# Kernel optimization log

Measured on AMD Instinct MI355X. Metric: run time of the kernel, lower is better.

## Reference

```python
import jax, jax.numpy as jnp
import numpy as np

SIGMA = 1.0

def setup_inputs() -> dict:
    key = jax.random.key(0)
    kx, ky = jax.random.split(key)
    x = jax.random.normal(kx, (8192, 256), dtype=jnp.float32)
    y = jax.random.normal(ky, (8192, 256), dtype=jnp.float32)
    return {"x": x, "y": y}

def reference(x, y):
    x2 = jnp.sum(x * x, axis=-1)            # [N]
    y2 = jnp.sum(y * y, axis=-1)            # [M]
    d2 = x2[:, None] + y2[None, :] - 2.0 * (x @ y.T)  # [N, M]
    d2 = jnp.maximum(d2, 0.0)
    k = jnp.exp(-d2 / (2.0 * SIGMA ** 2))
    # original: exp(...)[None].sum(dim=0).mean() == mean over all N*M entries
    return jnp.mean(k)
```

## Files before the change

### kernel.cpp

```cpp
#include <hip/hip_runtime.h>

#define NROWS 8192
#define DIM   256

typedef __bf16 bf16x8 __attribute__((ext_vector_type(8)));
typedef __bf16 bf16x4 __attribute__((ext_vector_type(4)));
typedef float  f32x4  __attribute__((ext_vector_type(4)));

typedef __attribute__((address_space(3))) char lds_char;
typedef __attribute__((address_space(1))) const char glob_char;

#define LOG2E  1.4426950408889634f
#define NEG_HALF_LOG2E (-0.7213475204444817f)

#define BAR() asm volatile("s_barrier" ::: "memory")

__global__ __launch_bounds__(256) void prep_kernel(
    const float* __restrict__ x, const float* __restrict__ y,
    __bf16* __restrict__ xb, __bf16* __restrict__ yb,
    float* __restrict__ px, float* __restrict__ py,
    float* __restrict__ out)
{
    int tid  = threadIdx.x;
    int lane = tid & 63;
    int w    = tid >> 6;
    int row  = blockIdx.x * 4 + w;
    bool isx = row < NROWS;
    int r    = isx ? row : row - NROWS;
    const float* src = (isx ? x : y) + (size_t)r * DIM;
    float4 v = reinterpret_cast<const float4*>(src)[lane];
    float sq = v.x*v.x + v.y*v.y + v.z*v.z + v.w*v.w;
    #pragma unroll
    for (int off = 32; off; off >>= 1) sq += __shfl_xor(sq, off);
    bf16x4 h;
    h[0] = (__bf16)v.x; h[1] = (__bf16)v.y; h[2] = (__bf16)v.z; h[3] = (__bf16)v.w;
    __bf16* dst = (isx ? xb : yb) + (size_t)r * DIM + lane * 4;
    *reinterpret_cast<bf16x4*>(dst) = h;
    if (lane == 0) (isx ? px : py)[r] = NEG_HALF_LOG2E * sq;
    if (blockIdx.x == 0 && tid == 0) out[0] = 0.0f;
}

__global__ __launch_bounds__(512, 1) void rbf_gemm_kernel(
    const __bf16* __restrict__ xb, const __bf16* __restrict__ yb,
    const float* __restrict__ px, const float* __restrict__ py,
    float* __restrict__ out)
{
    __shared__ char smem[131072];
    __shared__ float red[8];

    int tid  = threadIdx.x;
    int lane = tid & 63;
    int wv   = tid >> 6;
    int wm   = wv >> 2;
    int wn   = wv & 3;
    int bm   = blockIdx.x & 31;
    int bn   = blockIdx.x >> 5;
    int h    = lane >> 4;
    int l15  = lane & 15;

    f32x4 acc[8][4];
    #pragma unroll
    for (int m = 0; m < 8; ++m)
        #pragma unroll
        for (int n = 0; n < 4; ++n)
            acc[m][n] = (f32x4){0.f, 0.f, 0.f, 0.f};

    auto stage_unit = [&](int buf, int kt, int matrix, int unit) {
        const __bf16* src = matrix ? yb : xb;
        int baserow = (matrix ? bn : bm) * 256;
        #pragma unroll
        for (int j = 0; j < 2; ++j) {
            int lin = j * 8192 + tid * 16;
            int off;
            if (matrix == 0) off = unit * 8192 + lin + (lin >> 13) * 8192;
            else             off = unit * 4096 + lin + (lin >> 12) * 4096;
            int row = off >> 7;
            int kb  = off & 127;
            int kbs = kb ^ ((row & 7) << 4);
            size_t g = (size_t)(baserow + row) * 512 + (size_t)kt * 128 + kbs;
            __builtin_amdgcn_global_load_lds(
                (glob_char*)((const char*)src + g),
                (lds_char*)(smem + buf * 65536 + matrix * 32768 + off), 16, 0, 0);
        }
    };

    auto ldA = [&](int buf, int mbase, bf16x8* aF) {
        const char* Ab = smem + buf * 65536;
        #pragma unroll
        for (int m = 0; m < 4; ++m)
            #pragma unroll
            for (int kk = 0; kk < 2; ++kk) {
                int row = wm * 128 + (mbase + m) * 16 + l15;
                int kb  = (kk * 64 + h * 16) ^ ((row & 7) << 4);
                aF[m * 2 + kk] = *reinterpret_cast<const bf16x8*>(Ab + row * 128 + kb);
            }
    };
    auto ldB = [&](int buf, int nbase, bf16x8* bF) {
        const char* Bb = smem + buf * 65536 + 32768;
        #pragma unroll
        for (int n = 0; n < 2; ++n)
            #pragma unroll
            for (int kk = 0; kk < 2; ++kk) {
                int row = wn * 64 + (nbase + n) * 16 + l15;
                int kb  = (kk * 64 + h * 16) ^ ((row & 7) << 4);
                bF[n * 2 + kk] = *reinterpret_cast<const bf16x8*>(Bb + row * 128 + kb);
            }
    };
    auto mmaq = [&](int mbase, int nbase, bf16x8* aF, bf16x8* bF) {
        __builtin_amdgcn_s_setprio(1);
        #pragma unroll
        for (int m = 0; m < 4; ++m)
            #pragma unroll
            for (int n = 0; n < 2; ++n)
                #pragma unroll
                for (int kk = 0; kk < 2; ++kk)
                    acc[mbase + m][nbase + n] = __builtin_amdgcn_mfma_f32_16x16x32_bf16(
                        aF[m * 2 + kk], bF[n * 2 + kk], acc[mbase + m][nbase + n], 0, 0, 0);
        __builtin_amdgcn_s_setprio(0);
    };

    stage_unit(0, 0, 0, 0); stage_unit(0, 0, 1, 0);
    stage_unit(0, 0, 1, 1); stage_unit(0, 0, 0, 1);
    stage_unit(1, 1, 0, 0); stage_unit(1, 1, 1, 0);
    stage_unit(1, 1, 1, 1); stage_unit(1, 1, 0, 1);
    asm volatile("s_waitcnt vmcnt(8)" ::: "memory");
    BAR();

    #pragma unroll
    for (int kt = 0; kt < 4; ++kt) {
        int buf = kt & 1;
        bf16x8 aF[8], bF0[4], bF1[4];
        ldA(buf, 0, aF);
        ldB(buf, 0, bF0);
        mmaq(0, 0, aF, bF0);
        BAR();
        ldB(buf, 2, bF1);
        if (kt < 2) { stage_unit(buf, kt + 2, 0, 0); stage_unit(buf, kt + 2, 1, 0); }
        mmaq(0, 2, aF, bF1);
        BAR();
        ldA(buf, 4, aF);
        if (kt < 2) stage_unit(buf, kt + 2, 1, 1);
        mmaq(4, 2, aF, bF1);
        BAR();
        if (kt < 2) stage_unit(buf, kt + 2, 0, 1);
        mmaq(4, 0, aF, bF0);
        if (kt < 2)       asm volatile("s_waitcnt vmcnt(8)" ::: "memory");
        else if (kt == 2) asm volatile("s_waitcnt vmcnt(0)" ::: "memory");
        BAR();
    }

    float lsum = 0.f;
    int colbase = bn * 256 + wn * 64 + l15;
    int rowbase = bm * 256 + wm * 128 + h * 4;
    float py4[4];
    #pragma unroll
    for (int n = 0; n < 4; ++n) py4[n] = py[colbase + n * 16];
    #pragma unroll
    for (int m = 0; m < 8; ++m) {
        #pragma unroll
        for (int r = 0; r < 4; ++r) {
            float pxv = px[rowbase + m * 16 + r];
            #pragma unroll
            for (int n = 0; n < 4; ++n)
                lsum += exp2f(fmaf(acc[m][n][r], LOG2E, pxv + py4[n]));
        }
    }
    #pragma unroll
    for (int off = 32; off; off >>= 1) lsum += __shfl_xor(lsum, off);
    if (lane == 0) red[wv] = lsum;
    __syncthreads();
    if (tid == 0) {
        float s = (red[0] + red[1] + red[2] + red[3] +
                   red[4] + red[5] + red[6] + red[7]) * 1.4901161193847656e-08f;
        atomicAdd(out, s);
    }
}

extern "C" void kernel_launch(void* const* d_in, const int* in_sizes, int n_in,
                              void* d_out, int out_size, void* d_ws, size_t ws_size,
                              hipStream_t stream) {
    const float* x = (const float*)d_in[0];
    const float* y = (const float*)d_in[1];
    float* out = (float*)d_out;
    char* ws = (char*)d_ws;
    __bf16* xb = (__bf16*)ws;
    __bf16* yb = (__bf16*)(ws + (size_t)4 * 1024 * 1024);
    float*  px = (float*)(ws + (size_t)8 * 1024 * 1024);
    float*  py = (float*)(ws + (size_t)8 * 1024 * 1024 + 32 * 1024);

    hipLaunchKernelGGL(prep_kernel, dim3(4096), dim3(256), 0, stream,
                       x, y, xb, yb, px, py, out);
    hipLaunchKernelGGL(rbf_gemm_kernel, dim3(1024), dim3(512), 0, stream,
                       xb, yb, px, py, out);
}
```

Before: 113.5 us.

## Make GEMM blocks persistent over four N-tiles with cross-tile prefetch

Launches one block per CU (256 blocks), each looping over four consecutive 256-column output tiles for a fixed row block. Global-to-LDS staging of the next tile's first K slices overlaps with the current tile's last MFMA steps, hiding per-block prologue latency. The px/py norm vectors are preloaded into LDS via direct global-to-LDS loads and read vectorized in the epilogue. Epilogue exp work per tile is not overlapped with loads, and the added outer loop may raise register pressure.

```diff
diff --git a/kernel.cpp b/kernel.cpp
--- a/kernel.cpp
+++ b/kernel.cpp
@@ -45,18 +45,21 @@
     const float* __restrict__ px, const float* __restrict__ py,
     float* __restrict__ out)
 {
-    __shared__ char smem[131072];
-    __shared__ float red[8];
+    __shared__ __align__(16) char smem[136224];
+    float* pxl = (float*)(smem + 131072);
+    float* pyl = (float*)(smem + 132096);
+    float* red = (float*)(smem + 136192);
 
     int tid  = threadIdx.x;
     int lane = tid & 63;
     int wv   = tid >> 6;
     int wm   = wv >> 2;
     int wn   = wv & 3;
-    int bm   = blockIdx.x & 31;
-    int bn   = blockIdx.x >> 5;
+    int bm   = blockIdx.x >> 3;
+    int bng  = blockIdx.x & 7;
     int h    = lane >> 4;
     int l15  = lane & 15;
+    int arow = bm * 256;
 
     f32x4 acc[8][4];
     #pragma unroll
@@ -65,9 +68,8 @@
         for (int n = 0; n < 4; ++n)
             acc[m][n] = (f32x4){0.f, 0.f, 0.f, 0.f};
 
-    auto stage_unit = [&](int buf, int kt, int matrix, int unit) {
+    auto stage_unit = [&](int buf, int ktcol, int matrix, int unit, int baserow) {
         const __bf16* src = matrix ? yb : xb;
-        int baserow = (matrix ? bn : bm) * 256;
         #pragma unroll
         for (int j = 0; j < 2; ++j) {
             int lin = j * 8192 + tid * 16;
@@ -75,9 +77,8 @@
             if (matrix == 0) off = unit * 8192 + lin + (lin >> 13) * 8192;
             else             off = unit * 4096 + lin + (lin >> 12) * 4096;
             int row = off >> 7;
-            int kb  = off & 127;
-            int kbs = kb ^ ((row & 7) << 4);
-            size_t g = (size_t)(baserow + row) * 512 + (size_t)kt * 128 + kbs;
+            int kbs = (off & 127) ^ ((row & 7) << 4);
+            size_t g = (size_t)(baserow + row) * 512 + (size_t)ktcol + kbs;
             __builtin_amdgcn_global_load_lds(
                 (glob_char*)((const char*)src + g),
                 (lds_char*)(smem + buf * 65536 + matrix * 32768 + off), 16, 0, 0);
@@ -119,52 +120,73 @@
         __builtin_amdgcn_s_setprio(0);
     };
 
-    stage_unit(0, 0, 0, 0); stage_unit(0, 0, 1, 0);
-    stage_unit(0, 0, 1, 1); stage_unit(0, 0, 0, 1);
-    stage_unit(1, 1, 0, 0); stage_unit(1, 1, 1, 0);
-    stage_unit(1, 1, 1, 1); stage_unit(1, 1, 0, 1);
+    if (tid < 256)
+        __builtin_amdgcn_global_load_lds(
+            (glob_char*)((const char*)(px + arow) + tid * 4),
+            (lds_char*)((char*)pxl + tid * 4), 4, 0, 0);
+    #pragma unroll
+    for (int j = 0; j < 2; ++j)
+        __builtin_amdgcn_global_load_lds(
+            (glob_char*)((const char*)(py + bng * 1024) + j * 2048 + tid * 4),
+            (lds_char*)((char*)pyl + j * 2048 + tid * 4), 4, 0, 0);
+    int bn0row = bng * 4 * 256;
+    stage_unit(0, 0,   0, 0, arow); stage_unit(0, 0,   1, 0, bn0row);
+    stage_unit(0, 0,   1, 1, bn0row); stage_unit(0, 0,   0, 1, arow);
+    stage_unit(1, 128, 0, 0, arow); stage_unit(1, 128, 1, 0, bn0row);
+    stage_unit(1, 128, 1, 1, bn0row); stage_unit(1, 128, 0, 1, arow);
     asm volatile("s_waitcnt vmcnt(8)" ::: "memory");
     BAR();
 
-    #pragma unroll
-    for (int kt = 0; kt < 4; ++kt) {
-        int buf = kt & 1;
-        bf16x8 aF[8], bF0[4], bF1[4];
-        ldA(buf, 0, aF);
-        ldB(buf, 0, bF0);
-        mmaq(0, 0, aF, bF0);
-        BAR();
-        ldB(buf, 2, bF1);
-        if (kt < 2) { stage_unit(buf, kt + 2, 0, 0); stage_unit(buf, kt + 2, 1, 0); }
-        mmaq(0, 2, aF, bF1);
-        BAR();
-        ldA(buf, 4, aF);
-        if (kt < 2) stage_unit(buf, kt + 2, 1, 1);
-        mmaq(4, 2, aF, bF1);
-        BAR();
-        if (kt < 2) stage_unit(buf, kt + 2, 0, 1);
-        mmaq(4, 0, aF, bF0);
-        if (kt < 2)       asm volatile("s_waitcnt vmcnt(8)" ::: "memory");
-        else if (kt == 2) asm volatile("s_waitcnt vmcnt(0)" ::: "memory");
-        BAR();
-    }
-
     float lsum = 0.f;
-    int colbase = bn * 256 + wn * 64 + l15;
-    int rowbase = bm * 256 + wm * 128 + h * 4;
-    float py4[4];
-    #pragma unroll
-    for (int n = 0; n < 4; ++n) py4[n] = py[colbase + n * 16];
-    #pragma unroll
-    for (int m = 0; m < 8; ++m) {
-        #pragma unroll
-        for (int r = 0; r < 4; ++r) {
-            float pxv = px[rowbase + m * 16 + r];
+    for (int t = 0; t < 4; ++t) {
+        #pragma unroll
+        for (int kt = 0; kt < 4; ++kt) {
+            int buf = kt & 1;
+            bool st = (t < 3) || (kt < 2);
+            int tgt_kt  = (kt + 2) & 3;
+            int tgt_col = tgt_kt * 128;
+            int tgt_bnrow = (bng * 4 + t + (kt >> 1)) * 256;
+            bf16x8 aF[8], bF0[4], bF1[4];
+            ldA(buf, 0, aF);
+            ldB(buf, 0, bF0);
+            mmaq(0, 0, aF, bF0);
+            BAR();
+            ldB(buf, 2, bF1);
+            if (st) { stage_unit(buf, tgt_col, 0, 0, arow);
+                      stage_unit(buf, tgt_col, 1, 0, tgt_bnrow); }
+            mmaq(0, 2, aF, bF1);
+            BAR();
+            ldA(buf, 4, aF);
+            if (st) stage_unit(buf, tgt_col, 1, 1, tgt_bnrow);
+            mmaq(4, 2, aF, bF1);
+            BAR();
+            if (st) stage_unit(buf, tgt_col, 0, 1, arow);
+            mmaq(4, 0, aF, bF0);
+            if (st)            asm volatile("s_waitcnt vmcnt(8)" ::: "memory");
+            else if (kt == 2)  asm volatile("s_waitcnt vmcnt(0)" ::: "memory");
+            BAR();
+        }
+        float py4[4];
+        #pragma unroll
+        for (int n = 0; n < 4; ++n)
+            py4[n] = pyl[t * 256 + wn * 64 + n * 16 + l15];
+        #pragma unroll
+        for (int m = 0; m < 8; ++m) {
+            f32x4 pxm = *reinterpret_cast<const f32x4*>(
+                (const char*)pxl + (wm * 128 + m * 16 + h * 4) * 4);
+            #pragma unroll
+            for (int r = 0; r < 4; ++r) {
+                float pv = pxm[r];
+                #pragma unroll
+                for (int n = 0; n < 4; ++n)
+                    lsum += exp2f(fmaf(acc[m][n][r], LOG2E, pv + py4[n]));
+            }
             #pragma unroll
             for (int n = 0; n < 4; ++n)
-                lsum += exp2f(fmaf(acc[m][n][r], LOG2E, pxv + py4[n]));
+                acc[m][n] = (f32x4){0.f, 0.f, 0.f, 0.f};
         }
     }
+
     #pragma unroll
     for (int off = 32; off; off >>= 1) lsum += __shfl_xor(lsum, off);
     if (lane == 0) red[wv] = lsum;
@@ -190,6 +212,6 @@
 
     hipLaunchKernelGGL(prep_kernel, dim3(4096), dim3(256), 0, stream,
                        x, y, xb, yb, px, py, out);
-    hipLaunchKernelGGL(rbf_gemm_kernel, dim3(1024), dim3(512), 0, stream,
+    hipLaunchKernelGGL(rbf_gemm_kernel, dim3(256), dim3(512), 0, stream,
                        xb, yb, px, py, out);
 }
```

After: 152.5 us. 1.34x slower.
